# Optimization experiments

Hardware: AMD Instinct MI355X
Metric: run time of the kernel (lower is better)

The kernel has to match this reference:

```python
import jax, jax.numpy as jnp
import numpy as np

GAMMA = 0.7
ALPHA = 1.0
EPS = 1e-6

def setup_inputs() -> dict:
    key = jax.random.key(0)
    k1, k2 = jax.random.split(key)
    x = jax.random.normal(k1, (1, 4096, 1024), dtype=jnp.float32)
    attn = jax.random.uniform(k2, (1, 4096, 4096), dtype=jnp.float32)
    return {"x": x, "attn": attn, "layer_idx": 10, "total_layers": 12}


def reference(x, attn, layer_idx, total_layers):
    B, N, D = x.shape  # module's masking/cat logic requires B == 1
    if layer_idx < GAMMA * total_layers:
        return x

    # --- spatial autocorrelation score s ---
    a = x.mean(axis=-1)                                            # [B,N]
    z = (a - a.mean(1, keepdims=True)) / (a.std(1, ddof=1, keepdims=True) + EPS)
    # diag(z z^T * W) == z^2 * diag(W): skip the O(N^2) outer product
    I_l = z * z * jnp.diagonal(attn, axis1=-2, axis2=-1)           # [B,N]
    s = (I_l - I_l.mean(1, keepdims=True)) / (I_l.std(1, ddof=1, keepdims=True) + EPS)

    # --- threshold (torch.median returns the LOWER middle for even N) ---
    mu_s = s.mean(1, keepdims=True)
    abs_med = jnp.sort(jnp.abs(s), axis=1)[:, (N - 1) // 2][:, None]
    lb = ALPHA * (mu_s - abs_med)
    ub = ALPHA * (mu_s + abs_med)
    mask_A = (s < lb) | (s > ub)                                   # [B,N]

    xb = x[0]
    mA = mask_A[0]
    idx = jnp.arange(N)
    n_A = mA.sum()

    # compact A tokens to the front preserving original order
    orderA = jnp.argsort(~mA, stable=True)
    tokA = xb[orderA]                    # first n_A rows are tokens_A, rest are B tokens (masked later)
    mid = n_A // 2
    n2 = n_A - mid                       # number of A2 tokens

    # A1[i] = tokA[i] (valid i < mid); A2[j] = tokA[mid + j] (valid j < n2)
    A2 = jnp.take(tokA, jnp.clip(mid + idx, 0, N - 1), axis=0)     # [N,D] padded
    validA1 = idx < mid
    validA2 = idx < n2

    sim = tokA @ A2.T                                              # [N,N]
    sim = jnp.where(validA2[None, :], sim, -jnp.inf)
    matches = jnp.argmax(sim, axis=1)                              # [N]
    merged = 0.5 * (tokA + A2[matches])
    merged = jnp.where(validA1[:, None], merged, 0.0)              # rows >= mid zeroed

    # residual A2 tokens (not matched by any valid A1 row), compacted and zero-padded
    drop_idx = jnp.where(validA1, matches, N)                      # OOB index dropped
    matched = jnp.zeros(N, bool).at[drop_idx].set(True, mode='drop')
    resid_valid = validA2 & ~matched
    orderR = jnp.argsort(~resid_valid, stable=True)
    residual = jnp.where(resid_valid[orderR][:, None], A2[orderR], 0.0)  # [N,D]

    # B tokens compacted, then merged tokens appended, zero pad to N
    n_B = N - n_A
    orderB = jnp.argsort(mA, stable=True)
    tokB = jnp.where((idx < n_B)[:, None], xb[orderB], 0.0)        # [N,D]
    shift = jnp.clip(idx - n_B, 0, N - 1)
    in_merged = ((idx >= n_B) & (idx < n_B + mid)).astype(xb.dtype)[:, None]
    out = (tokB + in_merged * merged[shift])[None]                 # [1,N,D]
    return out, residual
```

## Files before the change

### kernel.cpp

```cpp
#include <hip/hip_runtime.h>

#define N 4096
#define D 1024
#define EPSF 1e-6f

typedef _Float16 f16;
typedef f16 f16x8 __attribute__((ext_vector_type(8)));
typedef float f32x4 __attribute__((ext_vector_type(4)));
typedef unsigned long long u64;

#define PLANE ((size_t)2048 * 1024)

struct WS {
  unsigned c1, c2, c3, c4;
  int n_A, mid, n2, n_B, n_resid, pad[3];
  float a[N];
  float diag[N];
  int A1idx[N];
  int A2idx[N];
  int Bidx[N];
  int matches[N];
  int residIdx[N];
  u64 bestKey[2048];
};

__device__ __forceinline__ u64 packKey(float v, int j) {
  unsigned u = __float_as_uint(v);
  unsigned m = (u & 0x80000000u) ? ~u : (u | 0x80000000u);
  return ((u64)m << 32) | (unsigned)(~(unsigned)j);
}

__global__ __launch_bounds__(1024) void k_pm(const float* __restrict__ x,
                                             const float* __restrict__ attn, WS* ws) {
  int tid = threadIdx.x;
  int lane = tid & 63, wv = tid >> 6;
  int bid = blockIdx.x;
  __shared__ int slast;

  {
    int row = bid * 16 + wv;
    const float4* xr = (const float4*)(x + (size_t)row * D);
    float sm = 0.f;
    #pragma unroll
    for (int it = 0; it < 4; it++) {
      float4 v = xr[it * 64 + lane];
      sm += v.x + v.y + v.z + v.w;
    }
    for (int o = 32; o; o >>= 1) sm += __shfl_down(sm, o, 64);
    if (lane == 0) {
      atomicExch((unsigned*)&ws->a[row], __float_as_uint(sm * (1.0f / D)));
      atomicExch((unsigned*)&ws->diag[row], __float_as_uint(attn[(size_t)row * (N + 1)]));
    }
  }
  __syncthreads();
  if (tid == 0) {
    unsigned c = atomicAdd(&ws->c1, 1u);
    slast = (c == 255u);
  }
  __syncthreads();
  if (!slast) return;

  __shared__ double dred[16], dred2[16];
  __shared__ float bcast[2];
  __shared__ int hist[256];
  __shared__ int wsum[16];
  __shared__ unsigned sPrefix;
  __shared__ int sRank;

  ws->bestKey[tid] = 0ull;
  ws->bestKey[tid + 1024] = 0ull;

  float av[4], dg[4];
  double s = 0.0, s2 = 0.0;
  #pragma unroll
  for (int q = 0; q < 4; q++) {
    int i = tid * 4 + q;
    av[q] = __uint_as_float(atomicOr((unsigned*)&ws->a[i], 0u));
    dg[q] = __uint_as_float(atomicOr((unsigned*)&ws->diag[i], 0u));
    s += av[q]; s2 += (double)av[q] * av[q];
  }
  for (int o = 32; o; o >>= 1) { s += __shfl_down(s, o, 64); s2 += __shfl_down(s2, o, 64); }
  if (lane == 0) { dred[wv] = s; dred2[wv] = s2; }
  __syncthreads();
  if (tid == 0) {
    double t1 = 0, t2 = 0;
    for (int i = 0; i < 16; i++) { t1 += dred[i]; t2 += dred2[i]; }
    bcast[0] = (float)(t1 / N);
    bcast[1] = (float)sqrt((t2 - t1 * t1 / N) / (N - 1));
  }
  __syncthreads();
  float meanA = bcast[0], stdA = bcast[1];

  float il[4];
  s = 0.0; s2 = 0.0;
  #pragma unroll
  for (int q = 0; q < 4; q++) {
    float z = (av[q] - meanA) / (stdA + EPSF);
    float I = z * z * dg[q];
    il[q] = I; s += I; s2 += (double)I * I;
  }
  for (int o = 32; o; o >>= 1) { s += __shfl_down(s, o, 64); s2 += __shfl_down(s2, o, 64); }
  __syncthreads();
  if (lane == 0) { dred[wv] = s; dred2[wv] = s2; }
  __syncthreads();
  if (tid == 0) {
    double t1 = 0, t2 = 0;
    for (int i = 0; i < 16; i++) { t1 += dred[i]; t2 += dred2[i]; }
    bcast[0] = (float)(t1 / N);
    bcast[1] = (float)sqrt((t2 - t1 * t1 / N) / (N - 1));
    sPrefix = 0u; sRank = (N - 1) / 2;
  }
  __syncthreads();
  float meanI = bcast[0], stdI = bcast[1];

  float sv[4]; unsigned ab[4];
  #pragma unroll
  for (int q = 0; q < 4; q++) {
    float sval = (il[q] - meanI) / (stdI + EPSF);
    sv[q] = sval;
    ab[q] = __float_as_uint(fabsf(sval));
  }

  for (int p = 3; p >= 0; p--) {
    if (tid < 256) hist[tid] = 0;
    __syncthreads();
    unsigned pre = sPrefix;
    int rk = sRank;
    int sh = p * 8;
    unsigned mHi = (p == 3) ? 0u : (0xFFFFFFFFu << (sh + 8));
    #pragma unroll
    for (int q = 0; q < 4; q++)
      if ((ab[q] & mHi) == pre) atomicAdd(&hist[(ab[q] >> sh) & 255], 1);
    __syncthreads();
    int v = (tid < 256) ? hist[tid] : 0;
    int inc = v;
    #pragma unroll
    for (int o = 1; o < 64; o <<= 1) { int u = __shfl_up(inc, o, 64); if (lane >= o) inc += u; }
    if (lane == 63) wsum[wv] = inc;
    __syncthreads();
    if (tid < 16) {
      int t = wsum[tid];
      #pragma unroll
      for (int o = 1; o < 16; o <<= 1) { int u = __shfl_up(t, o, 64); if (tid >= o) t += u; }
      wsum[tid] = t;
    }
    __syncthreads();
    int incl = (wv ? wsum[wv - 1] : 0) + inc;
    int E = incl - v;
    if (tid < 256 && v && rk >= E && rk < E + v) {
      sPrefix = pre | ((unsigned)tid << sh);
      sRank = rk - E;
    }
    __syncthreads();
  }
  float med = __uint_as_float(sPrefix);

  int msk[4], loc[4]; int tot = 0;
  #pragma unroll
  for (int q = 0; q < 4; q++) {
    bool m = fabsf(sv[q]) > med;
    msk[q] = m; loc[q] = tot; tot += (int)m;
  }
  int inc = tot;
  #pragma unroll
  for (int o = 1; o < 64; o <<= 1) { int u = __shfl_up(inc, o, 64); if (lane >= o) inc += u; }
  if (lane == 63) wsum[wv] = inc;
  __syncthreads();
  if (tid < 16) {
    int t = wsum[tid];
    #pragma unroll
    for (int o = 1; o < 16; o <<= 1) { int u = __shfl_up(t, o, 64); if (tid >= o) t += u; }
    wsum[tid] = t;
  }
  __syncthreads();
  int nA = wsum[15];
  int base = (wv ? wsum[wv - 1] : 0) + inc - tot;
  int midl = nA >> 1;
  #pragma unroll
  for (int q = 0; q < 4; q++) {
    int i = tid * 4 + q;
    int r = base + loc[q];
    if (msk[q]) {
      if (r < midl) ws->A1idx[r] = i; else ws->A2idx[r - midl] = i;
    } else {
      ws->Bidx[i - r] = i;
    }
  }
  if (tid == 0) { ws->n_A = nA; ws->mid = midl; ws->n2 = nA - midl; ws->n_B = N - nA; }
}

__global__ __launch_bounds__(128) void k_pack(const float* __restrict__ x,
                                              f16* __restrict__ PAhi, f16* __restrict__ PAlo,
                                              f16* __restrict__ PBhi, f16* __restrict__ PBlo,
                                              WS* ws) {
  int b = blockIdx.x, t = threadIdx.x;
  const float* src;
  f16 *dh, *dl;
  int j;
  if (b < 2048) {
    if (b >= ws->mid) return;
    j = b;
    src = x + (size_t)ws->A1idx[b] * D;
    dh = PAhi; dl = PAlo;
  } else {
    j = b - 2048;
    if (j >= ws->n2) return;
    src = x + (size_t)ws->A2idx[j] * D;
    dh = PBhi; dl = PBlo;
  }
  float4 v0 = ((const float4*)src)[t * 2];
  float4 v1 = ((const float4*)src)[t * 2 + 1];
  float vv[8] = {v0.x, v0.y, v0.z, v0.w, v1.x, v1.y, v1.z, v1.w};
  f16x8 h, l;
  #pragma unroll
  for (int q = 0; q < 8; q++) {
    f16 hq = (f16)vv[q];
    h[q] = hq;
    l[q] = (f16)(vv[q] - (float)hq);
  }
  int rt = j >> 6, rl = j & 63;
  int kt = t >> 3, gl = t & 7;
  size_t off = ((size_t)(rt * 16 + kt) << 12) + rl * 64 + ((gl ^ (rl & 7)) * 8);
  *(f16x8*)(dh + off) = h;
  *(f16x8*)(dl + off) = l;
}

__global__ __launch_bounds__(256) void k_gemm(const f16* __restrict__ PAhi,
                                              const f16* __restrict__ PAlo,
                                              const f16* __restrict__ PBhi,
                                              const f16* __restrict__ PBlo, WS* ws) {
  __shared__ __align__(16) f16 lds[2][4][64 * 64];
  __shared__ int isLast;

  const int mid = ws->mid, n2 = ws->n2;
  const int tid = threadIdx.x;
  const int lane = tid & 63;

  {
    int L = blockIdx.x;
    int local = L >> 3;
    int bj = ((L & 7) << 1) | (local >> 4);
    int bi = local & 15;
    if (bi * 64 < mid && bj * 64 < n2) {
      const int wid = tid >> 6;
      const int wr = wid >> 1, wc = wid & 1;
      const f16* plane = (wid == 0) ? PAhi : (wid == 1) ? PAlo : (wid == 2) ? PBhi : PBlo;
      const int ptile = (wid < 2) ? bi : bj;

      f16x8 pr[8];
      auto LOAD = [&](int t) {
        const f16* tb = plane + ((size_t)((ptile << 4) + t) << 12);
        #pragma unroll
        for (int i = 0; i < 8; i++) pr[i] = *(const f16x8*)(tb + i * 512 + lane * 8);
      };
      auto STORE = [&](int buf) {
        #pragma unroll
        for (int i = 0; i < 8; i++) *(f16x8*)&lds[buf][wid][i * 512 + lane * 8] = pr[i];
      };

      const int colg = lane & 15, rowg = lane >> 4;
      const int ma0 = wr * 32 + colg, ma1 = ma0 + 16;
      const int mb0 = wc * 32 + colg, mb1 = mb0 + 16;

      f32x4 zero = {0.f, 0.f, 0.f, 0.f};
      f32x4 acc[2][2];
      acc[0][0] = zero; acc[0][1] = zero; acc[1][0] = zero; acc[1][1] = zero;

#define FRAG(buf, t4, row, g) \
  (*(const f16x8*)&lds[buf][t4][(row) * 64 + ((((g) ^ ((row) & 7))) * 8)])

      LOAD(0);
      STORE(0);
      __syncthreads();
      #pragma unroll 1
      for (int t16 = 0; t16 < 16; t16++) {
        int buf = t16 & 1;
        if (t16 < 15) LOAD(t16 + 1);
        #pragma unroll
        for (int ks = 0; ks < 2; ks++) {
          int gk = ks * 4 + rowg;
          f16x8 ah0 = FRAG(buf, 0, ma0, gk), ah1 = FRAG(buf, 0, ma1, gk);
          f16x8 al0 = FRAG(buf, 1, ma0, gk), al1 = FRAG(buf, 1, ma1, gk);
          f16x8 bh0 = FRAG(buf, 2, mb0, gk), bh1 = FRAG(buf, 2, mb1, gk);
          f16x8 bl0 = FRAG(buf, 3, mb0, gk), bl1 = FRAG(buf, 3, mb1, gk);
          acc[0][0] = __builtin_amdgcn_mfma_f32_16x16x32_f16(ah0, bh0, acc[0][0], 0, 0, 0);
          acc[0][0] = __builtin_amdgcn_mfma_f32_16x16x32_f16(ah0, bl0, acc[0][0], 0, 0, 0);
          acc[0][0] = __builtin_amdgcn_mfma_f32_16x16x32_f16(al0, bh0, acc[0][0], 0, 0, 0);
          acc[0][1] = __builtin_amdgcn_mfma_f32_16x16x32_f16(ah0, bh1, acc[0][1], 0, 0, 0);
          acc[0][1] = __builtin_amdgcn_mfma_f32_16x16x32_f16(ah0, bl1, acc[0][1], 0, 0, 0);
          acc[0][1] = __builtin_amdgcn_mfma_f32_16x16x32_f16(al0, bh1, acc[0][1], 0, 0, 0);
          acc[1][0] = __builtin_amdgcn_mfma_f32_16x16x32_f16(ah1, bh0, acc[1][0], 0, 0, 0);
          acc[1][0] = __builtin_amdgcn_mfma_f32_16x16x32_f16(ah1, bl0, acc[1][0], 0, 0, 0);
          acc[1][0] = __builtin_amdgcn_mfma_f32_16x16x32_f16(al1, bh0, acc[1][0], 0, 0, 0);
          acc[1][1] = __builtin_amdgcn_mfma_f32_16x16x32_f16(ah1, bh1, acc[1][1], 0, 0, 0);
          acc[1][1] = __builtin_amdgcn_mfma_f32_16x16x32_f16(ah1, bl1, acc[1][1], 0, 0, 0);
          acc[1][1] = __builtin_amdgcn_mfma_f32_16x16x32_f16(al1, bh1, acc[1][1], 0, 0, 0);
        }
        if (t16 < 15) {
          __syncthreads();
          STORE(buf ^ 1);
          __syncthreads();
        }
      }
#undef FRAG

      #pragma unroll
      for (int mi = 0; mi < 2; mi++) {
        #pragma unroll
        for (int i = 0; i < 4; i++) {
          int grow = bi * 64 + wr * 32 + mi * 16 + rowg * 4 + i;
          u64 key = 0;
          #pragma unroll
          for (int ni = 0; ni < 2; ni++) {
            int gcol = bj * 64 + wc * 32 + ni * 16 + colg;
            if (gcol < n2) {
              u64 k2 = packKey(acc[mi][ni][i], gcol);
              if (k2 > key) key = k2;
            }
          }
          #pragma unroll
          for (int m = 8; m; m >>= 1) {
            u64 o = (u64)__shfl_xor((long long)key, m, 64);
            if (o > key) key = o;
          }
          if (colg == 0 && grow < mid && key) atomicMax(&ws->bestKey[grow], key);
        }
      }
    }
  }
  __syncthreads();
  if (tid == 0) {
    unsigned c = atomicAdd(&ws->c3, 1u);
    isLast = (c == 255u);
  }
  __syncthreads();
  if (!isLast) return;

  {
    int* flag = (int*)lds;
    int* mwsum = flag + N;
    int wv = tid >> 6;
    #pragma unroll
    for (int q = 0; q < 16; q++) flag[tid * 16 + q] = 0;
    __syncthreads();
    #pragma unroll
    for (int q = 0; q < 8; q++) {
      int r = tid + q * 256;
      if (r < mid) {
        u64 k = atomicMax(&ws->bestKey[r], 0ull);
        int j = (int)(~(unsigned)(k & 0xffffffffull));
        ws->matches[r] = j;
        flag[j] = 1;
      }
    }
    __syncthreads();
    int v[8], loc[8]; int tot = 0;
    #pragma unroll
    for (int q = 0; q < 8; q++) {
      int j = tid * 8 + q;
      bool val = (j < ws->n2) && (flag[j] == 0);
      v[q] = val; loc[q] = tot; tot += (int)val;
    }
    int inc = tot;
    #pragma unroll
    for (int o = 1; o < 64; o <<= 1) { int u = __shfl_up(inc, o, 64); if (lane >= o) inc += u; }
    if (lane == 63) mwsum[wv] = inc;
    __syncthreads();
    if (tid == 0) { mwsum[1] += mwsum[0]; mwsum[2] += mwsum[1]; mwsum[3] += mwsum[2]; }
    __syncthreads();
    int base = (wv ? mwsum[wv - 1] : 0) + inc - tot;
    #pragma unroll
    for (int q = 0; q < 8; q++)
      if (v[q]) ws->residIdx[base + loc[q]] = ws->A2idx[tid * 8 + q];
    if (tid == 0) ws->n_resid = mwsum[3];
  }
}

__global__ __launch_bounds__(256) void k_write(const float* __restrict__ x,
                                               float* __restrict__ out, WS* ws) {
  int r = blockIdx.x;
  int t = threadIdx.x;
  int n_B = ws->n_B, mid = ws->mid, n_resid = ws->n_resid;
  float4 res = make_float4(0.f, 0.f, 0.f, 0.f);
  if (r < N) {
    if (r < n_B) {
      res = ((const float4*)(x + (size_t)ws->Bidx[r] * D))[t];
    } else if (r < n_B + mid) {
      int m = r - n_B;
      float4 v1 = ((const float4*)(x + (size_t)ws->A1idx[m] * D))[t];
      float4 v2 = ((const float4*)(x + (size_t)ws->A2idx[ws->matches[m]] * D))[t];
      res = make_float4(0.5f * (v1.x + v2.x), 0.5f * (v1.y + v2.y),
                        0.5f * (v1.z + v2.z), 0.5f * (v1.w + v2.w));
    }
  } else {
    int k = r - N;
    if (k < n_resid) {
      res = ((const float4*)(x + (size_t)ws->residIdx[k] * D))[t];
    }
  }
  ((float4*)(out + (size_t)r * D))[t] = res;
}

extern "C" void kernel_launch(void* const* d_in, const int* in_sizes, int n_in,
                              void* d_out, int out_size, void* d_ws, size_t ws_size,
                              hipStream_t stream) {
  const float* x = (const float*)d_in[0];
  const float* attn = (const float*)d_in[1];
  float* out = (float*)d_out;
  WS* ws = (WS*)d_ws;
  f16* PAhi = (f16*)d_out;
  f16* PAlo = PAhi + PLANE;
  f16* PBhi = PAlo + PLANE;
  f16* PBlo = PBhi + PLANE;

  hipMemsetAsync(&ws->c1, 0, 4 * sizeof(unsigned), stream);
  k_pm<<<256, 1024, 0, stream>>>(x, attn, ws);
  k_pack<<<4096, 128, 0, stream>>>(x, PAhi, PAlo, PBhi, PBlo, ws);
  k_gemm<<<256, 256, 0, stream>>>(PAhi, PAlo, PBhi, PBlo, ws);
  k_write<<<2 * N, 256, 0, stream>>>(x, out, ws);
}
```

Baseline: 66.22 us.

## Split last-block reduction kernel into row-mean kernel plus single-block mask kernel

Replaces the fused k_pm kernel, which used an atomic counter so the last finishing block ran the global statistics, with two kernels: k_prep (one 256-thread block per row, computing the row mean and the diagonal element) and k_mask (one 1024-thread block for the statistics and masking). This drops the hipMemsetAsync launch, the atomic counter and the atomic loads and stores on the shared workspace. The c3 counter is now reset inside k_mask. The cost is one extra kernel launch and the boundary between the two kernels, in exchange for simpler code with more parallelism in the row reduction.

```diff
diff --git a/kernel.cpp b/kernel.cpp
--- a/kernel.cpp
+++ b/kernel.cpp
@@ -12,7 +12,7 @@
 #define PLANE ((size_t)2048 * 1024)
 
 struct WS {
-  unsigned c1, c2, c3, c4;
+  unsigned c3, pad0[3];
   int n_A, mid, n2, n_B, n_resid, pad[3];
   float a[N];
   float diag[N];
@@ -30,54 +30,42 @@
   return ((u64)m << 32) | (unsigned)(~(unsigned)j);
 }
 
-__global__ __launch_bounds__(1024) void k_pm(const float* __restrict__ x,
-                                             const float* __restrict__ attn, WS* ws) {
-  int tid = threadIdx.x;
-  int lane = tid & 63, wv = tid >> 6;
-  int bid = blockIdx.x;
-  __shared__ int slast;
-
-  {
-    int row = bid * 16 + wv;
-    const float4* xr = (const float4*)(x + (size_t)row * D);
-    float sm = 0.f;
-    #pragma unroll
-    for (int it = 0; it < 4; it++) {
-      float4 v = xr[it * 64 + lane];
-      sm += v.x + v.y + v.z + v.w;
-    }
-    for (int o = 32; o; o >>= 1) sm += __shfl_down(sm, o, 64);
-    if (lane == 0) {
-      atomicExch((unsigned*)&ws->a[row], __float_as_uint(sm * (1.0f / D)));
-      atomicExch((unsigned*)&ws->diag[row], __float_as_uint(attn[(size_t)row * (N + 1)]));
-    }
-  }
-  __syncthreads();
-  if (tid == 0) {
-    unsigned c = atomicAdd(&ws->c1, 1u);
-    slast = (c == 255u);
-  }
-  __syncthreads();
-  if (!slast) return;
-
+__global__ __launch_bounds__(256) void k_prep(const float* __restrict__ x,
+                                              const float* __restrict__ attn, WS* ws) {
+  int row = blockIdx.x;
+  int t = threadIdx.x;
+  float4 v = ((const float4*)(x + (size_t)row * D))[t];
+  float sm = v.x + v.y + v.z + v.w;
+  for (int o = 32; o; o >>= 1) sm += __shfl_down(sm, o, 64);
+  __shared__ float w[4];
+  if ((t & 63) == 0) w[t >> 6] = sm;
+  __syncthreads();
+  if (t == 0) {
+    ws->a[row] = (w[0] + w[1] + w[2] + w[3]) * (1.0f / D);
+    ws->diag[row] = attn[(size_t)row * N + row];
+  }
+}
+
+__global__ __launch_bounds__(1024) void k_mask(WS* ws) {
   __shared__ double dred[16], dred2[16];
   __shared__ float bcast[2];
   __shared__ int hist[256];
   __shared__ int wsum[16];
   __shared__ unsigned sPrefix;
   __shared__ int sRank;
+  int tid = threadIdx.x;
+  int lane = tid & 63, wv = tid >> 6;
 
   ws->bestKey[tid] = 0ull;
   ws->bestKey[tid + 1024] = 0ull;
-
-  float av[4], dg[4];
+  if (tid == 0) ws->c3 = 0u;
+
+  float av[4];
   double s = 0.0, s2 = 0.0;
   #pragma unroll
   for (int q = 0; q < 4; q++) {
-    int i = tid * 4 + q;
-    av[q] = __uint_as_float(atomicOr((unsigned*)&ws->a[i], 0u));
-    dg[q] = __uint_as_float(atomicOr((unsigned*)&ws->diag[i], 0u));
-    s += av[q]; s2 += (double)av[q] * av[q];
+    float f = ws->a[tid * 4 + q];
+    av[q] = f; s += f; s2 += (double)f * f;
   }
   for (int o = 32; o; o >>= 1) { s += __shfl_down(s, o, 64); s2 += __shfl_down(s2, o, 64); }
   if (lane == 0) { dred[wv] = s; dred2[wv] = s2; }
@@ -95,8 +83,9 @@
   s = 0.0; s2 = 0.0;
   #pragma unroll
   for (int q = 0; q < 4; q++) {
+    int i = tid * 4 + q;
     float z = (av[q] - meanA) / (stdA + EPSF);
-    float I = z * z * dg[q];
+    float I = z * z * ws->diag[i];
     il[q] = I; s += I; s2 += (double)I * I;
   }
   for (int o = 32; o; o >>= 1) { s += __shfl_down(s, o, 64); s2 += __shfl_down(s2, o, 64); }
@@ -413,8 +402,8 @@
   f16* PBhi = PAlo + PLANE;
   f16* PBlo = PBhi + PLANE;
 
-  hipMemsetAsync(&ws->c1, 0, 4 * sizeof(unsigned), stream);
-  k_pm<<<256, 1024, 0, stream>>>(x, attn, ws);
+  k_prep<<<N, 256, 0, stream>>>(x, attn, ws);
+  k_mask<<<1, 1024, 0, stream>>>(ws);
   k_pack<<<4096, 128, 0, stream>>>(x, PAhi, PAlo, PBhi, PBlo, ws);
   k_gemm<<<256, 256, 0, stream>>>(PAhi, PAlo, PBhi, PBlo, ws);
   k_write<<<2 * N, 256, 0, stream>>>(x, out, ws);
```

New measurement: 58.29 us. 12.0% less time.
